# Optimization experiments

Measured on AMD Instinct MI355X. Metric: run time of the kernel, lower is better.

The kernel has to match this reference:

```python
import jax, jax.numpy as jnp
import numpy as np

NUM_HEADS = 8
D_HEAD = 16
RY = RX = 2
PH = 2 * RY + 1
PW = 2 * RX + 1
P = PH * PW  # 25 spatial positions per patch


def setup_inputs() -> dict:
    key = jax.random.key(0)
    ks = jax.random.split(key, 7)
    B, T, H, W, C = 1, 3, 96, 96, 128
    Ck = NUM_HEADS * D_HEAD
    w = lambda k, shp: jax.random.normal(k, shp, jnp.float32) * 0.05
    return {
        "x": jax.random.normal(ks[0], (B, T, H, W, C), jnp.float32),
        "Wq": w(ks[1], (C, Ck)),
        "Wk": w(ks[2], (C, Ck)),
        "Wv": w(ks[3], (C, Ck)),
        "Wo": w(ks[4], (Ck, C)),
        "temp_emb": w(ks[5], (T, Ck)),
        "sp_emb": w(ks[6], (P, Ck)),
    }


def _neighbor_idx(N, r):
    # Edge handling: patch center is clipped into the valid interior, matching
    # extract_patches(VALID) + gather_nd with clipped indices in the original.
    c = jnp.clip(jnp.arange(N), r, N - r - 1)
    return c[:, None] + jnp.arange(-r, r + 1)[None, :]  # (N, 2r+1)


def _query_spatial_idx(H, W):
    # Position of each query pixel inside its (clipped) patch.
    yc = jnp.clip(jnp.arange(H), RY, H - RY - 1)
    xc = jnp.clip(jnp.arange(W), RX, W - RX - 1)
    yr = jnp.arange(H) - yc + RY  # (H,)
    xr = jnp.arange(W) - xc + RX  # (W,)
    return yr[:, None] * PW + xr[None, :]  # (H, W) in [0, P)


def reference(x, Wq, Wk, Wv, Wo, temp_emb, sp_emb):
    B, T, H, W, C = x.shape
    h, d = NUM_HEADS, D_HEAD
    Ck = h * d
    # 1x1 conv projections (no bias) == channel matmuls
    Q = jnp.einsum('bqyxc,ck->bqyxk', x, Wq)
    K = jnp.einsum('bqyxc,ck->bqyxk', x, Wk)
    V = jnp.einsum('bqyxc,ck->bqyxk', x, Wv)
    # positional encodings added AFTER projection (attention space)
    K = K + temp_emb[None, :, None, None, :]
    qidx = _query_spatial_idx(H, W)  # (H, W)
    Q = Q + temp_emb[None, :, None, None, :] + sp_emb[qidx][None, None]
    # local spatial patch extraction with clipped-edge handling
    ynb = _neighbor_idx(H, RY)  # (H, PH)
    xnb = _neighbor_idx(W, RX)  # (W, PW)
    Kp = K[:, :, ynb[:, None, :, None], xnb[None, :, None, :], :]  # (B,T,H,W,PH,PW,Ck)
    Vp = V[:, :, ynb[:, None, :, None], xnb[None, :, None, :], :]
    Kp = Kp.reshape(B, T, H, W, P, Ck) + sp_emb[None, None, None, None]
    Vp = Vp.reshape(B, T, H, W, P, Ck)
    # merge key time into the neighborhood axis: (B,H,W,T*P,h,d)
    Kn = Kp.transpose(0, 2, 3, 1, 4, 5).reshape(B, H, W, T * P, h, d)
    Vn = Vp.transpose(0, 2, 3, 1, 4, 5).reshape(B, H, W, T * P, h, d)
    Qh = Q.reshape(B, T, H, W, h, d)
    scale = 1.0 / jnp.sqrt(jnp.asarray(d, x.dtype))
    scores = jnp.einsum('bqyxnd,byxknd->bqyxnk', Qh, Kn) * scale
    attn = jax.nn.softmax(scores, axis=-1)  # over T*P neighborhood
    out = jnp.einsum('bqyxnk,byxknd->bqyxnd', attn, Vn).reshape(B, T, H, W, Ck)
    out = jnp.einsum('bqyxk,kc->bqyxc', out, Wo)  # output 1x1 conv
    # return_list=False -> concatenate the T outputs along channels
    return out.transpose(0, 2, 3, 1, 4).reshape(B, H, W, T * C)
```

## Files before the change

kernel.cpp:

```cpp
#include <hip/hip_runtime.h>
#include <hip/hip_bf16.h>
#include <math.h>

#define TT 3
#define HH 96
#define WWD 96
#define CCH 128
#define NROWS (TT*HH*WWD)

typedef __attribute__((ext_vector_type(8))) short short8;
typedef __attribute__((ext_vector_type(4))) short short4v;
typedef __attribute__((ext_vector_type(4))) float float4v;

__device__ __forceinline__ float bfu(unsigned short u){ union{unsigned u;float f;}c; c.u=((unsigned)u)<<16; return c.f; }
__device__ __forceinline__ unsigned short f2bf(float f){ __hip_bfloat16 h=__float2bfloat16(f); return *(unsigned short*)&h; }

#if defined(__has_builtin)
#if __has_builtin(__builtin_amdgcn_mfma_f32_16x16x16bf16_1k)
#define MFMA16(A,B,C) __builtin_amdgcn_mfma_f32_16x16x16bf16_1k(A,B,C,0,0,0)
#endif
#endif
#ifndef MFMA16
static __device__ __forceinline__ float4v mfma16_asm(short4v a, short4v b, float4v c){
    float4v d;
    asm("v_mfma_f32_16x16x16_bf16 %0, %1, %2, %3" : "=v"(d) : "v"(a), "v"(b), "v"(c));
    return d;
}
#define MFMA16(A,B,C) mfma16_asm(A,B,C)
#endif

__launch_bounds__(256)
__global__ void prep_kernel(const float* __restrict__ Wq, const float* __restrict__ Wk,
                            const float* __restrict__ Wv, const float* __restrict__ Wo,
                            unsigned short* __restrict__ Wt, unsigned short* __restrict__ Wo1,
                            unsigned short* __restrict__ Wo2) {
    __shared__ float ts[32][33];
    const int m = blockIdx.x >> 4, tile = blockIdx.x & 15;
    const int k0 = (tile >> 2) * 32, n0 = (tile & 3) * 32;
    const float* src = (m == 0) ? Wq : (m == 1) ? Wk : (m == 2) ? Wv : Wo;
    const int tid = threadIdx.x;
    const int c = tid & 31, r8 = tid >> 5;
#pragma unroll
    for (int rr = 0; rr < 4; ++rr) {
        int r = r8 * 4 + rr;
        ts[r][c] = src[(size_t)(k0 + r) * 128 + n0 + c];
    }
    __syncthreads();
#pragma unroll
    for (int rr = 0; rr < 4; ++rr) {
        int r = r8 * 4 + rr;
        float v = ts[c][r];
        if (m < 3) {
            Wt[(size_t)(m * 128 + n0 + r) * 128 + k0 + c] = f2bf(v);
        } else {
            unsigned short w1 = f2bf(v);
            Wo1[(size_t)(n0 + r) * 128 + k0 + c] = w1;
            Wo2[(size_t)(n0 + r) * 128 + k0 + c] = f2bf(v - bfu(w1));
        }
    }
}

__launch_bounds__(256)
__global__ void qkv_kernel(const float* __restrict__ x,
                           const unsigned short* __restrict__ Wt,
                           const float* __restrict__ temp_emb,
                           const float* __restrict__ sp_emb,
                           unsigned short* __restrict__ Qb,
                           unsigned short* __restrict__ Kb,
                           unsigned short* __restrict__ Vb) {
    __shared__ unsigned short xs[64 * 136];
    const int tid = threadIdx.x;
    const int q0 = blockIdx.x * 64;
    for (int e = tid; e < 2048; e += 256) {
        int row = e >> 5, col = (e & 31) * 4;
        float4 v = *(const float4*)(x + (size_t)(q0 + row) * CCH + col);
        ushort4 u; u.x = f2bf(v.x); u.y = f2bf(v.y); u.z = f2bf(v.z); u.w = f2bf(v.w);
        *(ushort4*)&xs[row * 136 + col] = u;
    }
    __syncthreads();
    const int w = tid >> 6, lane = tid & 63, quad = lane >> 4, l16 = lane & 15;
    float4v acc[6][4];
#pragma unroll
    for (int mt = 0; mt < 6; ++mt)
#pragma unroll
        for (int nt = 0; nt < 4; ++nt) acc[mt][nt] = (float4v){0,0,0,0};
#pragma unroll
    for (int ks = 0; ks < 4; ++ks) {
        short8 b[4];
#pragma unroll
        for (int nt = 0; nt < 4; ++nt)
            b[nt] = *(const short8*)&xs[(nt * 16 + l16) * 136 + ks * 32 + quad * 8];
#pragma unroll
        for (int mt = 0; mt < 6; ++mt) {
            short8 a = *(const short8*)(Wt + (size_t)(w * 96 + mt * 16 + l16) * CCH + ks * 32 + quad * 8);
#pragma unroll
            for (int nt = 0; nt < 4; ++nt)
                acc[mt][nt] = __builtin_amdgcn_mfma_f32_16x16x32_bf16(a, b[nt], acc[mt][nt], 0, 0, 0);
        }
    }
#pragma unroll
    for (int nt = 0; nt < 4; ++nt) {
        int q = q0 + nt * 16 + l16;
        int t = q / (HH * WWD); int rem = q - t * (HH * WWD);
        int yy = rem / WWD, xx = rem - (rem / WWD) * WWD;
        int qidx = (yy - min(max(yy, 2), 93) + 2) * 5 + (xx - min(max(xx, 2), 93) + 2);
#pragma unroll
        for (int mt = 0; mt < 6; ++mt) {
            int colc = w * 96 + mt * 16 + quad * 4;
            int mat = colc >> 7, colb = colc & 127;
            float4v a = acc[mt][nt];
            ushort4 u;
            if (mat == 0) {
                float4 te = *(const float4*)(temp_emb + t * CCH + colb);
                float4 se = *(const float4*)(sp_emb + qidx * CCH + colb);
                u.x = f2bf((a[0] + te.x + se.x) * 0.25f);
                u.y = f2bf((a[1] + te.y + se.y) * 0.25f);
                u.z = f2bf((a[2] + te.z + se.z) * 0.25f);
                u.w = f2bf((a[3] + te.w + se.w) * 0.25f);
                *(ushort4*)(Qb + (size_t)q * CCH + colb) = u;
            } else if (mat == 1) {
                float4 te = *(const float4*)(temp_emb + t * CCH + colb);
                u.x = f2bf(a[0] + te.x); u.y = f2bf(a[1] + te.y);
                u.z = f2bf(a[2] + te.z); u.w = f2bf(a[3] + te.w);
                *(ushort4*)(Kb + (size_t)q * CCH + colb) = u;
            } else {
                u.x = f2bf(a[0]); u.y = f2bf(a[1]); u.z = f2bf(a[2]); u.w = f2bf(a[3]);
                *(ushort4*)(Vb + (size_t)q * CCH + colb) = u;
            }
        }
    }
}

#define PX 4
#define WIN 8

__launch_bounds__(512, 4)
__global__ void attn_kernel(const unsigned short* Qb,
                            const unsigned short* __restrict__ Kb,
                            const unsigned short* __restrict__ Vb,
                            const float* __restrict__ sp_emb,
                            unsigned short* Ob) {
    __shared__ unsigned short Ks[64 * 136];
    __shared__ unsigned short Vt[128 * 68];
    __shared__ float biasL[8 * 3 * 25 * 17];

    const int tid = threadIdx.x;
    const int lane = tid & 63;
    const int w = tid >> 6;
    const int quad = lane >> 4, l16 = lane & 15;
    const int h16 = w * 16;

    const int bx = blockIdx.x % (WWD / PX);
    const int by = blockIdx.x / (WWD / PX);
    const int x0 = bx * PX, y0 = by * PX;
    const int xlo = min(max(x0 - 2, 0), WWD - WIN);
    const int ylo = min(max(y0 - 2, 0), HH - WIN);

    const int qdy = l16 >> 2, qdx = l16 & 3;
    const int yy = y0 + qdy, xx = x0 + qdx;
    const int yc = min(max(yy, 2), HH - 3), xc = min(max(xx, 2), WWD - 3);

    short4v qfr[3];
#pragma unroll
    for (int qt = 0; qt < 3; ++qt) {
        int qrow = qt * (HH * WWD) + yy * WWD + xx;
        qfr[qt] = *(const short4v*)(Qb + (size_t)qrow * CCH + h16 + quad * 4);
    }

    short4v sph[2], spl[2];
#pragma unroll
    for (int tile = 0; tile < 2; ++tile) {
        int kcr = min(tile * 16 + l16, 24);
        float4 v = *(const float4*)(sp_emb + (size_t)kcr * CCH + h16 + quad * 4);
        float vv[4] = {v.x, v.y, v.z, v.w};
        union { short4v s4; unsigned short u[4]; } ph, pl;
#pragma unroll
        for (int i = 0; i < 4; ++i) {
            ph.u[i] = f2bf(vv[i]);
            pl.u[i] = f2bf(vv[i] - bfu(ph.u[i]));
        }
        sph[tile] = ph.s4; spl[tile] = pl.s4;
    }

    const int bbase = w * (3 * 25 * 17);
#pragma unroll
    for (int qt = 0; qt < 3; ++qt) {
#pragma unroll
        for (int tile = 0; tile < 2; ++tile) {
            float4v d = MFMA16(spl[tile], qfr[qt], ((float4v){0.f,0.f,0.f,0.f}));
            d = MFMA16(sph[tile], qfr[qt], d);
#pragma unroll
            for (int r = 0; r < 4; ++r) {
                int kc = tile * 16 + quad * 4 + r;
                if (kc < 25) biasL[bbase + (qt * 25 + kc) * 17 + l16] = d[r];
            }
        }
    }

    int badr[16];
#pragma unroll
    for (int kt = 0; kt < 4; ++kt)
#pragma unroll
        for (int r = 0; r < 4; ++r) {
            int slot = kt * 16 + quad * 4 + r;
            int gy = ylo + (slot >> 3), gx = xlo + (slot & 7);
            int py = gy - yc + 2, px = gx - xc + 2;
            bool ok = (py >= 0) && (py < 5) && (px >= 0) && (px < 5);
            badr[kt * 4 + r] = ok ? (bbase + (py * 5 + px) * 17 + l16) : -1;
        }

    float m[3] = {-1e30f, -1e30f, -1e30f};
    float l[3] = {0.f, 0.f, 0.f};
    float4v oacc[3];
#pragma unroll
    for (int qt = 0; qt < 3; ++qt) oacc[qt] = (float4v){0.f,0.f,0.f,0.f};

    for (int t = 0; t < TT; ++t) {
        __syncthreads();
        for (int e = tid; e < 1024; e += 512) {
            int slot = e >> 4, c = e & 15;
            int gy = ylo + (slot >> 3), gx = xlo + (slot & 7);
            size_t g = ((size_t)(t * HH + gy) * WWD + gx) * CCH + c * 8;
            *(uint4*)&Ks[slot * 136 + c * 8] = *(const uint4*)(Kb + g);
        }
        for (int p = tid; p < 1024; p += 512) {
            int sp2 = p & 31, cq = p >> 5;
            int slot0 = sp2 * 2, ch0 = cq * 4;
            int gy = ylo + (slot0 >> 3), gx = xlo + (slot0 & 7);
            size_t g = ((size_t)(t * HH + gy) * WWD + gx) * CCH + ch0;
            uint2 a = *(const uint2*)(Vb + g);
            uint2 b = *(const uint2*)(Vb + g + CCH);
            unsigned v0 = (a.x & 0xffffu) | (b.x << 16);
            unsigned v1 = (a.x >> 16)     | (b.x & 0xffff0000u);
            unsigned v2 = (a.y & 0xffffu) | (b.y << 16);
            unsigned v3 = (a.y >> 16)     | (b.y & 0xffff0000u);
            *(unsigned*)&Vt[(ch0 + 0) * 68 + slot0] = v0;
            *(unsigned*)&Vt[(ch0 + 1) * 68 + slot0] = v1;
            *(unsigned*)&Vt[(ch0 + 2) * 68 + slot0] = v2;
            *(unsigned*)&Vt[(ch0 + 3) * 68 + slot0] = v3;
        }
        __syncthreads();

        short4v kfr[4], vfr[4];
#pragma unroll
        for (int kt = 0; kt < 4; ++kt) {
            kfr[kt] = *(const short4v*)&Ks[(kt * 16 + l16) * 136 + h16 + quad * 4];
            vfr[kt] = *(const short4v*)&Vt[(h16 + l16) * 68 + kt * 16 + quad * 4];
        }

#pragma unroll
        for (int qt = 0; qt < 3; ++qt) {
            float4v s[4];
#pragma unroll
            for (int kt = 0; kt < 4; ++kt) {
                float4v c;
#pragma unroll
                for (int r = 0; r < 4; ++r) {
                    int a = badr[kt * 4 + r];
                    c[r] = (a < 0) ? -1e30f : biasL[a + qt * 425];
                }
                s[kt] = MFMA16(kfr[kt], qfr[qt], c);
            }
            float mx = m[qt];
#pragma unroll
            for (int kt = 0; kt < 4; ++kt)
#pragma unroll
                for (int r = 0; r < 4; ++r) mx = fmaxf(mx, s[kt][r]);
            mx = fmaxf(mx, __shfl_xor(mx, 16));
            mx = fmaxf(mx, __shfl_xor(mx, 32));
            float corr = __expf(m[qt] - mx);
            m[qt] = mx;
            l[qt] *= corr;
            float4v oc = oacc[qt] * corr;
            float lsum = 0.f;
            short4v pfr[4];
#pragma unroll
            for (int kt = 0; kt < 4; ++kt) {
                float p0 = __expf(s[kt][0] - mx), p1 = __expf(s[kt][1] - mx);
                float p2 = __expf(s[kt][2] - mx), p3 = __expf(s[kt][3] - mx);
                lsum += (p0 + p1) + (p2 + p3);
                union { short4v s4; unsigned short u[4]; } pk;
                pk.u[0] = f2bf(p0); pk.u[1] = f2bf(p1);
                pk.u[2] = f2bf(p2); pk.u[3] = f2bf(p3);
                pfr[kt] = pk.s4;
            }
            l[qt] += lsum;
#pragma unroll
            for (int kt = 0; kt < 4; ++kt) oc = MFMA16(vfr[kt], pfr[kt], oc);
            oacc[qt] = oc;
        }
    }

#pragma unroll
    for (int qt = 0; qt < 3; ++qt) {
        float lt = l[qt];
        lt += __shfl_xor(lt, 16);
        lt += __shfl_xor(lt, 32);
        float inv = 1.f / lt;
        union { ushort4 u4; unsigned short u[4]; } ob;
#pragma unroll
        for (int r = 0; r < 4; ++r) ob.u[r] = f2bf(oacc[qt][r] * inv);
        int qrow = qt * (HH * WWD) + yy * WWD + xx;
        *(ushort4*)(Ob + (size_t)qrow * CCH + h16 + quad * 4) = ob.u4;
    }
}

__launch_bounds__(256)
__global__ void out_proj_kernel(const unsigned short* __restrict__ A,
                                const unsigned short* __restrict__ Wo1,
                                const unsigned short* __restrict__ Wo2,
                                float* __restrict__ out) {
    __shared__ unsigned short as[64 * 136];
    const int tid = threadIdx.x;
    const int q0 = blockIdx.x * 64;
    for (int e = tid; e < 1024; e += 256) {
        int row = e >> 4, c = e & 15;
        *(uint4*)&as[row * 136 + c * 8] = *(const uint4*)(A + (size_t)(q0 + row) * CCH + c * 8);
    }
    __syncthreads();
    const int w = tid >> 6, lane = tid & 63, quad = lane >> 4, l16 = lane & 15;
    float4v acc[2][4];
#pragma unroll
    for (int mt = 0; mt < 2; ++mt)
#pragma unroll
        for (int nt = 0; nt < 4; ++nt) acc[mt][nt] = (float4v){0,0,0,0};
#pragma unroll
    for (int ks = 0; ks < 4; ++ks) {
        short8 b[4];
#pragma unroll
        for (int nt = 0; nt < 4; ++nt)
            b[nt] = *(const short8*)&as[(nt * 16 + l16) * 136 + ks * 32 + quad * 8];
#pragma unroll
        for (int mt = 0; mt < 2; ++mt) {
            size_t wo = (size_t)(w * 32 + mt * 16 + l16) * CCH + ks * 32 + quad * 8;
            short8 a1 = *(const short8*)(Wo1 + wo);
            short8 a2 = *(const short8*)(Wo2 + wo);
#pragma unroll
            for (int nt = 0; nt < 4; ++nt) {
                acc[mt][nt] = __builtin_amdgcn_mfma_f32_16x16x32_bf16(a1, b[nt], acc[mt][nt], 0, 0, 0);
                acc[mt][nt] = __builtin_amdgcn_mfma_f32_16x16x32_bf16(a2, b[nt], acc[mt][nt], 0, 0, 0);
            }
        }
    }
#pragma unroll
    for (int nt = 0; nt < 4; ++nt) {
        int q = q0 + nt * 16 + l16;
        int t = q / (HH * WWD); int rem = q - t * (HH * WWD);
        int yy = rem / WWD, xx = rem - (rem / WWD) * WWD;
        size_t ob = ((size_t)(yy * WWD + xx) * TT + t) * CCH;
#pragma unroll
        for (int mt = 0; mt < 2; ++mt) {
            float4 o;
            o.x = acc[mt][nt][0]; o.y = acc[mt][nt][1];
            o.z = acc[mt][nt][2]; o.w = acc[mt][nt][3];
            *(float4*)(out + ob + w * 32 + mt * 16 + quad * 4) = o;
        }
    }
}

extern "C" void kernel_launch(void* const* d_in, const int* in_sizes, int n_in,
                              void* d_out, int out_size, void* d_ws, size_t ws_size,
                              hipStream_t stream) {
    const float* x        = (const float*)d_in[0];
    const float* Wq       = (const float*)d_in[1];
    const float* Wk       = (const float*)d_in[2];
    const float* Wv       = (const float*)d_in[3];
    const float* Wo       = (const float*)d_in[4];
    const float* temp_emb = (const float*)d_in[5];
    const float* sp_emb   = (const float*)d_in[6];
    float* out = (float*)d_out;

    const size_t nb = (size_t)NROWS * CCH * 2;
    unsigned short* Qb  = (unsigned short*)d_ws;
    unsigned short* Kb  = (unsigned short*)((char*)d_ws + nb);
    unsigned short* Vb  = (unsigned short*)((char*)d_ws + 2 * nb);
    unsigned short* Wt  = (unsigned short*)((char*)d_ws + 3 * nb);
    unsigned short* Wo1 = Wt + 384 * 128;
    unsigned short* Wo2 = Wo1 + 128 * 128;

    prep_kernel<<<64, 256, 0, stream>>>(Wq, Wk, Wv, Wo, Wt, Wo1, Wo2);
    qkv_kernel<<<NROWS / 64, 256, 0, stream>>>(x, Wt, temp_emb, sp_emb, Qb, Kb, Vb);
    attn_kernel<<<(HH / PX) * (WWD / PX), 512, 0, stream>>>(Qb, Kb, Vb, sp_emb, Qb);
    out_proj_kernel<<<NROWS / 64, 256, 0, stream>>>(Qb, Wo1, Wo2, out);
}
```

Measured before the change: 145.4 us.

## Fuse output projection into attention kernel and halve QKV block rows

The output 1x1 projection is moved into the attention kernel. Each block stages its normalized bf16 attention output (3 time steps x 16 pixels x 128 channels) in shared memory, reusing the K buffer, then runs the split-bf16 Wo MFMA and writes the fp32 result directly. This removes the intermediate attention-output round trip through global memory and one kernel launch. The QKV kernel is also retiled to 32 rows per block to double the block count, at the cost of fewer MFMAs reusing each weight load.

```diff
diff --git a/kernel.cpp b/kernel.cpp
--- a/kernel.cpp
+++ b/kernel.cpp
@@ -68,10 +68,10 @@
                            unsigned short* __restrict__ Qb,
                            unsigned short* __restrict__ Kb,
                            unsigned short* __restrict__ Vb) {
-    __shared__ unsigned short xs[64 * 136];
+    __shared__ unsigned short xs[32 * 136];
     const int tid = threadIdx.x;
-    const int q0 = blockIdx.x * 64;
-    for (int e = tid; e < 2048; e += 256) {
+    const int q0 = blockIdx.x * 32;
+    for (int e = tid; e < 1024; e += 256) {
         int row = e >> 5, col = (e & 31) * 4;
         float4 v = *(const float4*)(x + (size_t)(q0 + row) * CCH + col);
         ushort4 u; u.x = f2bf(v.x); u.y = f2bf(v.y); u.z = f2bf(v.z); u.w = f2bf(v.w);
@@ -79,27 +79,27 @@
     }
     __syncthreads();
     const int w = tid >> 6, lane = tid & 63, quad = lane >> 4, l16 = lane & 15;
-    float4v acc[6][4];
+    float4v acc[6][2];
 #pragma unroll
     for (int mt = 0; mt < 6; ++mt)
 #pragma unroll
-        for (int nt = 0; nt < 4; ++nt) acc[mt][nt] = (float4v){0,0,0,0};
+        for (int nt = 0; nt < 2; ++nt) acc[mt][nt] = (float4v){0,0,0,0};
 #pragma unroll
     for (int ks = 0; ks < 4; ++ks) {
-        short8 b[4];
-#pragma unroll
-        for (int nt = 0; nt < 4; ++nt)
+        short8 b[2];
+#pragma unroll
+        for (int nt = 0; nt < 2; ++nt)
             b[nt] = *(const short8*)&xs[(nt * 16 + l16) * 136 + ks * 32 + quad * 8];
 #pragma unroll
         for (int mt = 0; mt < 6; ++mt) {
             short8 a = *(const short8*)(Wt + (size_t)(w * 96 + mt * 16 + l16) * CCH + ks * 32 + quad * 8);
 #pragma unroll
-            for (int nt = 0; nt < 4; ++nt)
+            for (int nt = 0; nt < 2; ++nt)
                 acc[mt][nt] = __builtin_amdgcn_mfma_f32_16x16x32_bf16(a, b[nt], acc[mt][nt], 0, 0, 0);
         }
     }
 #pragma unroll
-    for (int nt = 0; nt < 4; ++nt) {
+    for (int nt = 0; nt < 2; ++nt) {
         int q = q0 + nt * 16 + l16;
         int t = q / (HH * WWD); int rem = q - t * (HH * WWD);
         int yy = rem / WWD, xx = rem - (rem / WWD) * WWD;
@@ -135,11 +135,13 @@
 #define WIN 8
 
 __launch_bounds__(512, 4)
-__global__ void attn_kernel(const unsigned short* Qb,
+__global__ void attn_kernel(const unsigned short* __restrict__ Qb,
                             const unsigned short* __restrict__ Kb,
                             const unsigned short* __restrict__ Vb,
                             const float* __restrict__ sp_emb,
-                            unsigned short* Ob) {
+                            const unsigned short* __restrict__ Wo1,
+                            const unsigned short* __restrict__ Wo2,
+                            float* __restrict__ out) {
     __shared__ unsigned short Ks[64 * 136];
     __shared__ unsigned short Vt[128 * 68];
     __shared__ float biasL[8 * 3 * 25 * 17];
@@ -291,6 +293,8 @@
         }
     }
 
+    __syncthreads();
+    unsigned short* Os = Ks;
 #pragma unroll
     for (int qt = 0; qt < 3; ++qt) {
         float lt = l[qt];
@@ -300,61 +304,34 @@
         union { ushort4 u4; unsigned short u[4]; } ob;
 #pragma unroll
         for (int r = 0; r < 4; ++r) ob.u[r] = f2bf(oacc[qt][r] * inv);
-        int qrow = qt * (HH * WWD) + yy * WWD + xx;
-        *(ushort4*)(Ob + (size_t)qrow * CCH + h16 + quad * 4) = ob.u4;
-    }
-}
-
-__launch_bounds__(256)
-__global__ void out_proj_kernel(const unsigned short* __restrict__ A,
-                                const unsigned short* __restrict__ Wo1,
-                                const unsigned short* __restrict__ Wo2,
-                                float* __restrict__ out) {
-    __shared__ unsigned short as[64 * 136];
-    const int tid = threadIdx.x;
-    const int q0 = blockIdx.x * 64;
-    for (int e = tid; e < 1024; e += 256) {
-        int row = e >> 4, c = e & 15;
-        *(uint4*)&as[row * 136 + c * 8] = *(const uint4*)(A + (size_t)(q0 + row) * CCH + c * 8);
+        *(ushort4*)&Os[(qt * 16 + l16) * 136 + h16 + quad * 4] = ob.u4;
     }
     __syncthreads();
-    const int w = tid >> 6, lane = tid & 63, quad = lane >> 4, l16 = lane & 15;
-    float4v acc[2][4];
-#pragma unroll
-    for (int mt = 0; mt < 2; ++mt)
-#pragma unroll
-        for (int nt = 0; nt < 4; ++nt) acc[mt][nt] = (float4v){0,0,0,0};
+
+    float4v pacc[3];
+#pragma unroll
+    for (int nt = 0; nt < 3; ++nt) pacc[nt] = (float4v){0.f, 0.f, 0.f, 0.f};
 #pragma unroll
     for (int ks = 0; ks < 4; ++ks) {
-        short8 b[4];
-#pragma unroll
-        for (int nt = 0; nt < 4; ++nt)
-            b[nt] = *(const short8*)&as[(nt * 16 + l16) * 136 + ks * 32 + quad * 8];
-#pragma unroll
-        for (int mt = 0; mt < 2; ++mt) {
-            size_t wo = (size_t)(w * 32 + mt * 16 + l16) * CCH + ks * 32 + quad * 8;
-            short8 a1 = *(const short8*)(Wo1 + wo);
-            short8 a2 = *(const short8*)(Wo2 + wo);
-#pragma unroll
-            for (int nt = 0; nt < 4; ++nt) {
-                acc[mt][nt] = __builtin_amdgcn_mfma_f32_16x16x32_bf16(a1, b[nt], acc[mt][nt], 0, 0, 0);
-                acc[mt][nt] = __builtin_amdgcn_mfma_f32_16x16x32_bf16(a2, b[nt], acc[mt][nt], 0, 0, 0);
-            }
-        }
-    }
-#pragma unroll
-    for (int nt = 0; nt < 4; ++nt) {
-        int q = q0 + nt * 16 + l16;
-        int t = q / (HH * WWD); int rem = q - t * (HH * WWD);
-        int yy = rem / WWD, xx = rem - (rem / WWD) * WWD;
-        size_t ob = ((size_t)(yy * WWD + xx) * TT + t) * CCH;
-#pragma unroll
-        for (int mt = 0; mt < 2; ++mt) {
-            float4 o;
-            o.x = acc[mt][nt][0]; o.y = acc[mt][nt][1];
-            o.z = acc[mt][nt][2]; o.w = acc[mt][nt][3];
-            *(float4*)(out + ob + w * 32 + mt * 16 + quad * 4) = o;
-        }
+        short8 bfrag[3];
+#pragma unroll
+        for (int nt = 0; nt < 3; ++nt)
+            bfrag[nt] = *(const short8*)&Os[(nt * 16 + l16) * 136 + ks * 32 + quad * 8];
+        size_t wo = (size_t)(w * 16 + l16) * CCH + ks * 32 + quad * 8;
+        short8 a1 = *(const short8*)(Wo1 + wo);
+        short8 a2 = *(const short8*)(Wo2 + wo);
+#pragma unroll
+        for (int nt = 0; nt < 3; ++nt) {
+            pacc[nt] = __builtin_amdgcn_mfma_f32_16x16x32_bf16(a1, bfrag[nt], pacc[nt], 0, 0, 0);
+            pacc[nt] = __builtin_amdgcn_mfma_f32_16x16x32_bf16(a2, bfrag[nt], pacc[nt], 0, 0, 0);
+        }
+    }
+#pragma unroll
+    for (int nt = 0; nt < 3; ++nt) {
+        size_t ob = ((size_t)(yy * WWD + xx) * TT + nt) * CCH;
+        float4 o;
+        o.x = pacc[nt][0]; o.y = pacc[nt][1]; o.z = pacc[nt][2]; o.w = pacc[nt][3];
+        *(float4*)(out + ob + w * 16 + quad * 4) = o;
     }
 }
 
@@ -379,7 +356,6 @@
     unsigned short* Wo2 = Wo1 + 128 * 128;
 
     prep_kernel<<<64, 256, 0, stream>>>(Wq, Wk, Wv, Wo, Wt, Wo1, Wo2);
-    qkv_kernel<<<NROWS / 64, 256, 0, stream>>>(x, Wt, temp_emb, sp_emb, Qb, Kb, Vb);
-    attn_kernel<<<(HH / PX) * (WWD / PX), 512, 0, stream>>>(Qb, Kb, Vb, sp_emb, Qb);
-    out_proj_kernel<<<NROWS / 64, 256, 0, stream>>>(Qb, Wo1, Wo2, out);
-}
+    qkv_kernel<<<NROWS / 32, 256, 0, stream>>>(x, Wt, temp_emb, sp_emb, Qb, Kb, Vb);
+    attn_kernel<<<(HH / PX) * (WWD / PX), 512, 0, stream>>>(Qb, Kb, Vb, sp_emb, Wo1, Wo2, out);
+}
```

Result: no change. 144.8 us (-0.4%).
